# Kernel tuning notes

Hardware: AMD Instinct MI355X
Metric: run time of the kernel (lower is better)

## Reference

```python
import jax, jax.numpy as jnp
import numpy as np

V, D, NL, NC = 16, 256, 4, 2
MAXL, NSTATE, DCONV, EXPAND, HEADDIM = 1024, 64, 4, 2, 64
DIN = EXPAND * D            # 512 inner channels
H = DIN // HEADDIM          # 8 heads
P = HEADDIM                 # 64 head dim
CONV_DIM = DIN + 2 * NSTATE # 640 channels through depthwise conv
D_IN_PROJ = 2 * DIN + 2 * NSTATE + H  # 1160
B_, L_ = 2, 1024
EPS = 1e-5


def setup_inputs() -> dict:
    key = jax.random.key(0)
    ks = iter(jax.random.split(key, 32))

    def rn(shape, s=0.02):
        return jax.random.normal(next(ks), shape, jnp.float32) * s

    emb = rn((V, D)).at[4].set(0.0)  # padding_idx=4 row zeroed
    pos_emb = rn((MAXL, D))
    in_proj_w = rn((NL, D_IN_PROJ, D))
    conv_w = rn((NL, CONV_DIM, DCONV), 0.1)
    conv_b = rn((NL, CONV_DIM), 0.1)
    dt_bias = rn((NL, H), 0.5)
    A_log = jnp.log(jax.random.uniform(next(ks), (NL, H), jnp.float32, 1.0, 16.0))
    D_param = jnp.ones((NL, H), jnp.float32)
    norm_w = jnp.ones((NL, DIN), jnp.float32)
    out_proj_w = rn((NL, D, DIN))
    pooler_w = rn((D, D), 0.05)
    pooler_b = jnp.zeros((D,), jnp.float32)
    cls1_w = rn((D // 2, D), 0.05)
    cls1_b = jnp.zeros((D // 2,), jnp.float32)
    cls2_w = rn((NC, D // 2), 0.05)
    cls2_b = jnp.zeros((NC,), jnp.float32)
    input_ids = jax.random.randint(next(ks), (B_, L_), 0, V)
    return dict(input_ids=input_ids, emb=emb, pos_emb=pos_emb,
                in_proj_w=in_proj_w, conv_w=conv_w, conv_b=conv_b,
                dt_bias=dt_bias, A_log=A_log, D_param=D_param, norm_w=norm_w,
                out_proj_w=out_proj_w, pooler_w=pooler_w, pooler_b=pooler_b,
                cls1_w=cls1_w, cls1_b=cls1_b, cls2_w=cls2_w, cls2_b=cls2_b)


def _mamba2(x, Win, cw, cb, dtb, A_log, Dp, nw, Wout):
    Bsz, L, _ = x.shape
    zxbcdt = jnp.einsum('bld,pd->blp', x, Win)              # (B,L,2*DIN+2N+H)
    z = zxbcdt[..., :DIN]
    xBC = zxbcdt[..., DIN:DIN + CONV_DIM]
    dt = jax.nn.softplus(zxbcdt[..., -H:] + dtb)            # (B,L,H)
    # causal depthwise conv over time
    xBC = jnp.transpose(xBC, (0, 2, 1))                     # (B,C,L)
    xBC = jax.lax.conv_general_dilated(
        xBC, cw[:, None, :], (1,), [(DCONV - 1, 0)],
        dimension_numbers=('NCH', 'OIH', 'NCH'),
        feature_group_count=CONV_DIM)
    xBC = jax.nn.silu(jnp.transpose(xBC, (0, 2, 1)) + cb)   # (B,L,C)
    xs = xBC[..., :DIN].reshape(Bsz, L, H, P)
    Bm = xBC[..., DIN:DIN + NSTATE]                         # (B,L,N)
    Cm = xBC[..., DIN + NSTATE:]                            # (B,L,N)
    A = -jnp.exp(A_log)                                     # (H,)
    dA = jnp.exp(dt * A)                                    # (B,L,H)
    dBx = dt[..., None, None] * xs[..., None] * Bm[:, :, None, None, :]  # (B,L,H,P,N)

    def step(h, inp):
        dA_t, dBx_t, C_t = inp
        h = dA_t[:, :, None, None] * h + dBx_t              # (B,H,P,N)
        y = jnp.einsum('bhpn,bn->bhp', h, C_t)
        return h, y

    h0 = jnp.zeros((Bsz, H, P, NSTATE), x.dtype)
    _, y = jax.lax.scan(step, h0, (jnp.moveaxis(dA, 1, 0),
                                   jnp.moveaxis(dBx, 1, 0),
                                   jnp.moveaxis(Cm, 1, 0)))
    y = jnp.moveaxis(y, 0, 1) + Dp[None, None, :, None] * xs  # (B,L,H,P)
    y = y.reshape(Bsz, L, DIN) * jax.nn.silu(z)               # gated
    y = y * jax.lax.rsqrt(jnp.mean(y * y, axis=-1, keepdims=True) + EPS) * nw
    return jnp.einsum('bld,od->blo', y, Wout)


def reference(input_ids, emb, pos_emb, in_proj_w, conv_w, conv_b, dt_bias,
              A_log, D_param, norm_w, out_proj_w, pooler_w, pooler_b,
              cls1_w, cls1_b, cls2_w, cls2_b):
    L = input_ids.shape[1]
    x = emb[input_ids] + pos_emb[:L][None]                  # (B,L,D)
    for i in range(NL):
        x = x + _mamba2(x, in_proj_w[i], conv_w[i], conv_b[i], dt_bias[i],
                        A_log[i], D_param[i], norm_w[i], out_proj_w[i])
    pooled = (x.mean(axis=1) + x.max(axis=1)) * 0.5         # (B,D)
    pooled = jax.nn.gelu(pooled @ pooler_w.T + pooler_b, approximate=False)
    hcls = jax.nn.gelu(pooled @ cls1_w.T + cls1_b, approximate=False)
    return hcls @ cls2_w.T + cls2_b
```

## Files before the change

### kernel.cpp

```cpp
#include <hip/hip_runtime.h>
#include <math.h>

#define D_ 256
#define NL_ 4
#define NC_ 2
#define L_LEN 1024
#define NSTATE_ 64
#define DIN_ 512
#define H_ 8
#define P_ 64
#define CONVDIM_ 640
#define DPROJ_ 1160
#define EPS_ 1e-5f
#define NCH_ 16

typedef __attribute__((ext_vector_type(8))) short short8;
typedef __attribute__((ext_vector_type(4))) float f32x4;
typedef __attribute__((ext_vector_type(4))) unsigned short us4;

__device__ __forceinline__ float siluf(float x) { return x / (1.f + __expf(-x)); }
__device__ __forceinline__ float geluf(float x) { return 0.5f * x * (1.f + erff(x * 0.70710678118654752f)); }
__device__ __forceinline__ unsigned short f2bf(float f) {
    unsigned u = __float_as_uint(f);
    u += 0x7FFFu + ((u >> 16) & 1u);
    return (unsigned short)(u >> 16);
}
__device__ __forceinline__ float bf2f(unsigned short h) {
    return __uint_as_float(((unsigned)h) << 16);
}

__global__ void k_embed(const int* __restrict__ ids, const float* __restrict__ emb,
                        const float* __restrict__ pos, float* __restrict__ x, int total) {
    int i = blockIdx.x * blockDim.x + threadIdx.x;
    if (i >= total) return;
    int d = i & (D_ - 1);
    int bl = i >> 8;
    int l = bl & (L_LEN - 1);
    x[i] = emb[ids[bl] * D_ + d] + pos[l * D_ + d];
}

__global__ void k_w2bf2(const float* __restrict__ Wi, const float* __restrict__ Wo,
                        const float* __restrict__ nw,
                        unsigned short* __restrict__ wih, unsigned short* __restrict__ wil,
                        unsigned short* __restrict__ woh, unsigned short* __restrict__ wol,
                        int nin, int ntot) {
    int i = blockIdx.x * blockDim.x + threadIdx.x;
    if (i >= ntot) return;
    if (i < nin) {
        float f = Wi[i];
        unsigned short h = f2bf(f);
        wih[i] = h;
        wil[i] = f2bf(f - bf2f(h));
    } else {
        int j = i - nin;
        int layer = j / (D_ * DIN_);
        int k = j % DIN_;
        float f = Wo[j] * nw[layer * DIN_ + k];
        unsigned short h = f2bf(f);
        woh[j] = h;
        wol[j] = f2bf(f - bf2f(h));
    }
}

__global__ void __launch_bounds__(256) gemm_in(const float* __restrict__ A,
        const unsigned short* __restrict__ Bhi, const unsigned short* __restrict__ Blo,
        float* __restrict__ C, int M, int N, int K) {
    __shared__ __align__(16) unsigned short Ah[128 * 40];
    __shared__ __align__(16) unsigned short Al[128 * 40];
    __shared__ __align__(16) unsigned short Bh[64 * 40];
    __shared__ __align__(16) unsigned short Bl[64 * 40];
    const int tid = threadIdx.x;
    const int col0 = blockIdx.x * 64;
    const int row0 = blockIdx.y * 128;

    const int sar = tid >> 1, sas = (tid & 1) * 16;
    const int sbr = tid >> 2, sbs = (tid & 3) * 8;
    const bool bok = (col0 + sbr) < N;
    const float* aptr = A + (size_t)(row0 + sar) * K + sas;
    const unsigned short* bhptr = Bhi + (size_t)(col0 + sbr) * K + sbs;
    const unsigned short* blptr = Blo + (size_t)(col0 + sbr) * K + sbs;

    float4 pa[4];
    short8 pbh = {0, 0, 0, 0, 0, 0, 0, 0}, pbl = {0, 0, 0, 0, 0, 0, 0, 0};
#pragma unroll
    for (int i = 0; i < 4; ++i) pa[i] = *(const float4*)(aptr + i * 4);
    if (bok) {
        pbh = *(const short8*)bhptr;
        pbl = *(const short8*)blptr;
    }

    const int wave = tid >> 6, lane = tid & 63;
    const int lq = lane >> 4, lm = lane & 15;
    f32x4 acc[2][4] = {};
    const int nsteps = K >> 5;
    for (int s = 0; s < nsteps; ++s) {
        __syncthreads();
#pragma unroll
        for (int i = 0; i < 4; ++i) {
            float4 f = pa[i];
            unsigned short h0 = f2bf(f.x), h1 = f2bf(f.y), h2 = f2bf(f.z), h3 = f2bf(f.w);
            us4 hv = {h0, h1, h2, h3};
            us4 lv = {f2bf(f.x - bf2f(h0)), f2bf(f.y - bf2f(h1)),
                      f2bf(f.z - bf2f(h2)), f2bf(f.w - bf2f(h3))};
            *(us4*)&Ah[sar * 40 + sas + i * 4] = hv;
            *(us4*)&Al[sar * 40 + sas + i * 4] = lv;
        }
        *(short8*)&Bh[sbr * 40 + sbs] = pbh;
        *(short8*)&Bl[sbr * 40 + sbs] = pbl;
        __syncthreads();
        if (s + 1 < nsteps) {
            int ko = (s + 1) * 32;
#pragma unroll
            for (int i = 0; i < 4; ++i) pa[i] = *(const float4*)(aptr + ko + i * 4);
            if (bok) {
                pbh = *(const short8*)(bhptr + ko);
                pbl = *(const short8*)(blptr + ko);
            }
        }
        short8 bh[4], bl[4];
#pragma unroll
        for (int ct = 0; ct < 4; ++ct) {
            bh[ct] = *(const short8*)&Bh[(ct * 16 + lm) * 40 + lq * 8];
            bl[ct] = *(const short8*)&Bl[(ct * 16 + lm) * 40 + lq * 8];
        }
#pragma unroll
        for (int rt = 0; rt < 2; ++rt) {
            short8 ah = *(const short8*)&Ah[(wave * 32 + rt * 16 + lm) * 40 + lq * 8];
            short8 al = *(const short8*)&Al[(wave * 32 + rt * 16 + lm) * 40 + lq * 8];
#pragma unroll
            for (int ct = 0; ct < 4; ++ct) {
                acc[rt][ct] = __builtin_amdgcn_mfma_f32_16x16x32_bf16(ah, bh[ct], acc[rt][ct], 0, 0, 0);
                acc[rt][ct] = __builtin_amdgcn_mfma_f32_16x16x32_bf16(ah, bl[ct], acc[rt][ct], 0, 0, 0);
                acc[rt][ct] = __builtin_amdgcn_mfma_f32_16x16x32_bf16(al, bh[ct], acc[rt][ct], 0, 0, 0);
            }
        }
    }
#pragma unroll
    for (int rt = 0; rt < 2; ++rt) {
#pragma unroll
        for (int ct = 0; ct < 4; ++ct) {
            int col = col0 + ct * 16 + lm;
            if (col >= N) continue;
            int rbase = row0 + wave * 32 + rt * 16 + lq * 4;
#pragma unroll
            for (int reg = 0; reg < 4; ++reg) {
                C[(size_t)(rbase + reg) * N + col] = acc[rt][ct][reg];
            }
        }
    }
}

__global__ void __launch_bounds__(256) gemm_outs(const unsigned short* __restrict__ Ghg,
        const unsigned short* __restrict__ Glg, const float* __restrict__ rowssq,
        const unsigned short* __restrict__ Bhi, const unsigned short* __restrict__ Blo,
        float* __restrict__ x) {
    __shared__ __align__(16) unsigned short Ah[128 * 40];
    __shared__ __align__(16) unsigned short Al[128 * 40];
    __shared__ __align__(16) unsigned short Bh[64 * 40];
    __shared__ __align__(16) unsigned short Bl[64 * 40];
    const int tid = threadIdx.x;
    const int col0 = blockIdx.x * 64;
    const int row0 = blockIdx.y * 128;
    const int kbase = blockIdx.z * 128;
    const int sar = tid >> 1, sas = (tid & 1) * 16;
    const int sbr = tid >> 2, sbs = (tid & 3) * 8;
    const unsigned short* ahptr = Ghg + (size_t)(row0 + sar) * DIN_ + kbase + sas;
    const unsigned short* alptr = Glg + (size_t)(row0 + sar) * DIN_ + kbase + sas;
    const unsigned short* bhptr = Bhi + (size_t)(col0 + sbr) * DIN_ + kbase + sbs;
    const unsigned short* blptr = Blo + (size_t)(col0 + sbr) * DIN_ + kbase + sbs;

    short8 pah0 = *(const short8*)ahptr, pah1 = *(const short8*)(ahptr + 8);
    short8 pal0 = *(const short8*)alptr, pal1 = *(const short8*)(alptr + 8);
    short8 pbh = *(const short8*)bhptr, pbl = *(const short8*)blptr;

    const int wave = tid >> 6, lane = tid & 63;
    const int lq = lane >> 4, lm = lane & 15;
    f32x4 acc[2][4] = {};
    for (int s = 0; s < 4; ++s) {
        __syncthreads();
        *(short8*)&Ah[sar * 40 + sas] = pah0;
        *(short8*)&Ah[sar * 40 + sas + 8] = pah1;
        *(short8*)&Al[sar * 40 + sas] = pal0;
        *(short8*)&Al[sar * 40 + sas + 8] = pal1;
        *(short8*)&Bh[sbr * 40 + sbs] = pbh;
        *(short8*)&Bl[sbr * 40 + sbs] = pbl;
        __syncthreads();
        if (s + 1 < 4) {
            int ko = (s + 1) * 32;
            pah0 = *(const short8*)(ahptr + ko);
            pah1 = *(const short8*)(ahptr + ko + 8);
            pal0 = *(const short8*)(alptr + ko);
            pal1 = *(const short8*)(alptr + ko + 8);
            pbh = *(const short8*)(bhptr + ko);
            pbl = *(const short8*)(blptr + ko);
        }
        short8 bh[4], bl[4];
#pragma unroll
        for (int ct = 0; ct < 4; ++ct) {
            bh[ct] = *(const short8*)&Bh[(ct * 16 + lm) * 40 + lq * 8];
            bl[ct] = *(const short8*)&Bl[(ct * 16 + lm) * 40 + lq * 8];
        }
#pragma unroll
        for (int rt = 0; rt < 2; ++rt) {
            short8 ah = *(const short8*)&Ah[(wave * 32 + rt * 16 + lm) * 40 + lq * 8];
            short8 al = *(const short8*)&Al[(wave * 32 + rt * 16 + lm) * 40 + lq * 8];
#pragma unroll
            for (int ct = 0; ct < 4; ++ct) {
                acc[rt][ct] = __builtin_amdgcn_mfma_f32_16x16x32_bf16(ah, bh[ct], acc[rt][ct], 0, 0, 0);
                acc[rt][ct] = __builtin_amdgcn_mfma_f32_16x16x32_bf16(ah, bl[ct], acc[rt][ct], 0, 0, 0);
                acc[rt][ct] = __builtin_amdgcn_mfma_f32_16x16x32_bf16(al, bh[ct], acc[rt][ct], 0, 0, 0);
            }
        }
    }
#pragma unroll
    for (int rt = 0; rt < 2; ++rt) {
        int rbase = row0 + wave * 32 + rt * 16 + lq * 4;
        float sc[4];
#pragma unroll
        for (int reg = 0; reg < 4; ++reg)
            sc[reg] = rsqrtf(rowssq[rbase + reg] * (1.f / DIN_) + EPS_);
#pragma unroll
        for (int ct = 0; ct < 4; ++ct) {
            int col = col0 + ct * 16 + lm;
#pragma unroll
            for (int reg = 0; reg < 4; ++reg) {
                atomicAdd(&x[(size_t)(rbase + reg) * D_ + col], sc[reg] * acc[rt][ct][reg]);
            }
        }
    }
}

__global__ void __launch_bounds__(512) k_ssmA(const float* __restrict__ zx,
        const float* __restrict__ cw, const float* __restrict__ cb,
        const float* __restrict__ dtbias, const float* __restrict__ Alog,
        const float* __restrict__ Dp,
        float* __restrict__ Sbuf, float* __restrict__ decay,
        float* __restrict__ Ctil, float* __restrict__ y, float* __restrict__ rowssq) {
    __shared__ float U[64][65];
    __shared__ float V[64][65];
    __shared__ float W[64][65];
    __shared__ float sdt[64], cs[64], wj[64];
    const int c = blockIdx.x, bh = blockIdx.y;
    const int b = bh >> 3, h = bh & 7;
    const int l0 = c << 6;
    const int tid = threadIdx.x, wid8 = tid >> 6, lane = tid & 63;

    if (h == 0 && tid < 64) rowssq[b * L_LEN + l0 + tid] = 0.f;

    const int chx = h * P_ + lane;
    const int chb = DIN_ + lane;
    const int chc = DIN_ + NSTATE_ + lane;
    float wx0 = cw[chx * 4], wx1 = cw[chx * 4 + 1], wx2 = cw[chx * 4 + 2], wx3 = cw[chx * 4 + 3];
    float wb0 = cw[chb * 4], wb1 = cw[chb * 4 + 1], wb2 = cw[chb * 4 + 2], wb3 = cw[chb * 4 + 3];
    float wc0 = cw[chc * 4], wc1 = cw[chc * 4 + 1], wc2 = cw[chc * 4 + 2], wc3 = cw[chc * 4 + 3];
    float bx = cb[chx], bb = cb[chb], bc = cb[chc];

    for (int r = 0; r < 64; r += 8) {
        int j = r + wid8;
        int l = l0 + j;
        float ax = bx, ab = bb, ac = bc;
#pragma unroll
        for (int k = 0; k < 4; ++k) {
            int t = l - 3 + k;
            if (t >= 0) {
                const float* row = zx + (size_t)(b * L_LEN + t) * DPROJ_;
                float wxk = (k == 0) ? wx0 : (k == 1) ? wx1 : (k == 2) ? wx2 : wx3;
                float wbk = (k == 0) ? wb0 : (k == 1) ? wb1 : (k == 2) ? wb2 : wb3;
                float wck = (k == 0) ? wc0 : (k == 1) ? wc1 : (k == 2) ? wc2 : wc3;
                ax += wxk * row[DIN_ + chx];
                ab += wbk * row[DIN_ + chb];
                ac += wck * row[DIN_ + chc];
            }
        }
        U[j][lane] = siluf(ax);
        V[j][lane] = siluf(ab);
        W[j][lane] = siluf(ac);
    }
    if (tid < 64) {
        float xv = zx[(size_t)(b * L_LEN + l0 + tid) * DPROJ_ + (DPROJ_ - H_) + h] + dtbias[h];
        float sp = fmaxf(xv, 0.f) + log1pf(__expf(-fabsf(xv)));
        sdt[tid] = sp;
        float v = sp * (-__expf(Alog[h]));
#pragma unroll
        for (int off = 1; off < 64; off <<= 1) {
            float t = __shfl_up(v, off, 64);
            if (tid >= off) v += t;
        }
        cs[tid] = v;
        float tot = __shfl(v, 63, 64);
        wj[tid] = __expf(tot - v) * sp;
        if (tid == 63) decay[bh * NCH_ + c] = __expf(tot);
    }
    __syncthreads();

    const int t4 = (tid & 15) * 4;
    const int r4 = ((tid >> 4) & 15) * 4;
    const size_t sbase = (size_t)(bh * NCH_ + c) * 4096;

    if (tid < 256) {
        float acc[4][4] = {};
        for (int j = 0; j < 64; ++j) {
            float w = wj[j];
            float4 xv = *(const float4*)&U[j][r4];
            float4 bv = *(const float4*)&V[j][t4];
            float xw[4] = {xv.x * w, xv.y * w, xv.z * w, xv.w * w};
#pragma unroll
            for (int ii = 0; ii < 4; ++ii) {
                acc[ii][0] += xw[ii] * bv.x;
                acc[ii][1] += xw[ii] * bv.y;
                acc[ii][2] += xw[ii] * bv.z;
                acc[ii][3] += xw[ii] * bv.w;
            }
        }
#pragma unroll
        for (int ii = 0; ii < 4; ++ii) {
            float4 v = {acc[ii][0], acc[ii][1], acc[ii][2], acc[ii][3]};
            *(float4*)&Sbuf[sbase + (size_t)(r4 + ii) * 64 + t4] = v;
        }
    }
    for (int r = 0; r < 64; r += 8) {
        int ii = r + wid8;
        Ctil[sbase + ii * 64 + lane] = __expf(cs[ii]) * W[ii][lane];
    }
    float wt[4][4];
    if (tid < 256) {
        float g[4][4] = {};
        for (int ng = 0; ng < 64; ng += 4) {
            float4 cf[4], bf[4];
#pragma unroll
            for (int ii = 0; ii < 4; ++ii) cf[ii] = *(const float4*)&W[r4 + ii][ng];
#pragma unroll
            for (int jj = 0; jj < 4; ++jj) bf[jj] = *(const float4*)&V[t4 + jj][ng];
#pragma unroll
            for (int ii = 0; ii < 4; ++ii)
#pragma unroll
                for (int jj = 0; jj < 4; ++jj)
                    g[ii][jj] += cf[ii].x * bf[jj].x + cf[ii].y * bf[jj].y +
                                 cf[ii].z * bf[jj].z + cf[ii].w * bf[jj].w;
        }
#pragma unroll
        for (int ii = 0; ii < 4; ++ii) {
            int i = r4 + ii;
            float csi = cs[i];
#pragma unroll
            for (int jj = 0; jj < 4; ++jj) {
                int j = t4 + jj;
                wt[ii][jj] = (j <= i) ? __expf(fminf(csi - cs[j], 0.f)) * sdt[j] * g[ii][jj] : 0.f;
            }
        }
    }
    __syncthreads();
    if (tid < 256) {
#pragma unroll
        for (int jj = 0; jj < 4; ++jj) {
            float4 v = {wt[0][jj], wt[1][jj], wt[2][jj], wt[3][jj]};
            *(float4*)&V[t4 + jj][r4] = v;
        }
    }
    __syncthreads();
    if (tid < 256) {
        float acc[4][4] = {};
        for (int j = 0; j < 64; ++j) {
            float4 wv = *(const float4*)&V[j][r4];
            float4 xv = *(const float4*)&U[j][t4];
            float ws[4] = {wv.x, wv.y, wv.z, wv.w};
#pragma unroll
            for (int ii = 0; ii < 4; ++ii) {
                acc[ii][0] += ws[ii] * xv.x;
                acc[ii][1] += ws[ii] * xv.y;
                acc[ii][2] += ws[ii] * xv.z;
                acc[ii][3] += ws[ii] * xv.w;
            }
        }
        float Dh = Dp[h];
#pragma unroll
        for (int ii = 0; ii < 4; ++ii) {
            float4 xv = *(const float4*)&U[r4 + ii][t4];
            float4 v = {acc[ii][0] + Dh * xv.x, acc[ii][1] + Dh * xv.y,
                        acc[ii][2] + Dh * xv.z, acc[ii][3] + Dh * xv.w};
            *(float4*)&y[(size_t)(b * L_LEN + l0 + r4 + ii) * DIN_ + h * P_ + t4] = v;
        }
    }
}

__global__ void __launch_bounds__(512) k_inter(const float* __restrict__ Sbuf,
        const float* __restrict__ Ctil, const float* __restrict__ decay,
        const float* __restrict__ zx, const float* __restrict__ y,
        unsigned short* __restrict__ gh, unsigned short* __restrict__ gl,
        float* __restrict__ rowssq) {
    __shared__ float Sm[64][65];
    __shared__ float Cm[64][65];
    const int c = blockIdx.x, bh = blockIdx.y;
    const int b = bh >> 3, h = bh & 7;
    const int l0 = c << 6;
    const int tid = threadIdx.x, wid8 = tid >> 6, lane = tid & 63;
    const size_t bhbase = (size_t)bh * NCH_ * 4096;

    float dec[NCH_];
#pragma unroll
    for (int k = 0; k < NCH_; ++k) dec[k] = decay[bh * NCH_ + k];

    float acc8[8] = {};
    float wgt = 1.f;
    for (int cp = c - 1; cp >= 0; --cp) {
        const float* src = Sbuf + bhbase + (size_t)cp * 4096;
#pragma unroll
        for (int i = 0; i < 8; ++i) acc8[i] += wgt * src[i * 512 + tid];
        wgt *= dec[cp];
    }
#pragma unroll
    for (int i = 0; i < 8; ++i) Sm[i * 8 + wid8][lane] = acc8[i];

    const size_t base = bhbase + (size_t)c * 4096;
    for (int r = 0; r < 64; r += 8) {
        int pp = r + wid8;
        Cm[pp][lane] = Ctil[base + pp * 64 + lane];
    }
    __syncthreads();
    const int t4 = (tid & 15) * 4;
    const int r4 = ((tid >> 4) & 15) * 4;
    if (tid < 256) {
        float acc[4][4] = {};
        if (c > 0) {
            for (int ng = 0; ng < 64; ng += 4) {
                float4 cf[4], sf[4];
#pragma unroll
                for (int ii = 0; ii < 4; ++ii) cf[ii] = *(const float4*)&Cm[r4 + ii][ng];
#pragma unroll
                for (int pp = 0; pp < 4; ++pp) sf[pp] = *(const float4*)&Sm[t4 + pp][ng];
#pragma unroll
                for (int ii = 0; ii < 4; ++ii)
#pragma unroll
                    for (int pp = 0; pp < 4; ++pp)
                        acc[ii][pp] += cf[ii].x * sf[pp].x + cf[ii].y * sf[pp].y +
                                       cf[ii].z * sf[pp].z + cf[ii].w * sf[pp].w;
            }
        }
        float ssq[4];
#pragma unroll
        for (int ii = 0; ii < 4; ++ii) {
            int row = b * L_LEN + l0 + r4 + ii;
            const float* yr = &y[(size_t)row * DIN_ + h * P_ + t4];
            const float* zr = &zx[(size_t)row * DPROJ_ + h * P_ + t4];
            float4 v = *(const float4*)yr;
            float4 z = *(const float4*)zr;
            v.x = (v.x + acc[ii][0]) * siluf(z.x);
            v.y = (v.y + acc[ii][1]) * siluf(z.y);
            v.z = (v.z + acc[ii][2]) * siluf(z.z);
            v.w = (v.w + acc[ii][3]) * siluf(z.w);
            unsigned short h0 = f2bf(v.x), h1 = f2bf(v.y), h2 = f2bf(v.z), h3 = f2bf(v.w);
            us4 hv = {h0, h1, h2, h3};
            us4 lv = {f2bf(v.x - bf2f(h0)), f2bf(v.y - bf2f(h1)),
                      f2bf(v.z - bf2f(h2)), f2bf(v.w - bf2f(h3))};
            *(us4*)&gh[(size_t)row * DIN_ + h * P_ + t4] = hv;
            *(us4*)&gl[(size_t)row * DIN_ + h * P_ + t4] = lv;
            ssq[ii] = v.x * v.x + v.y * v.y + v.z * v.z + v.w * v.w;
        }
#pragma unroll
        for (int o = 1; o < 16; o <<= 1) {
#pragma unroll
            for (int ii = 0; ii < 4; ++ii) ssq[ii] += __shfl_xor(ssq[ii], o, 64);
        }
        if ((tid & 15) == 0) {
#pragma unroll
            for (int ii = 0; ii < 4; ++ii)
                atomicAdd(&rowssq[b * L_LEN + l0 + r4 + ii], ssq[ii]);
        }
    }
}

__global__ void __launch_bounds__(1024) k_poolhead(const float* __restrict__ x,
                           const float* __restrict__ pw, const float* __restrict__ pb,
                           const float* __restrict__ c1w, const float* __restrict__ c1b,
                           const float* __restrict__ c2w, const float* __restrict__ c2b,
                           float* __restrict__ out) {
    __shared__ float ps[4][256], pm[4][256];
    __shared__ float sp[256], s1[256], s2[128];
    int b = blockIdx.x, tid = threadIdx.x;
    int t = tid & 255, grp = tid >> 8;
    const float* xb = x + (size_t)b * L_LEN * D_ + (size_t)grp * 256 * D_ + t;
    float s = 0.f, m = -INFINITY;
    for (int l = 0; l < 256; l += 4) {
        float v0 = xb[(size_t)l * D_];
        float v1 = xb[(size_t)(l + 1) * D_];
        float v2 = xb[(size_t)(l + 2) * D_];
        float v3 = xb[(size_t)(l + 3) * D_];
        s += v0 + v1 + v2 + v3;
        m = fmaxf(m, fmaxf(fmaxf(v0, v1), fmaxf(v2, v3)));
    }
    ps[grp][t] = s;
    pm[grp][t] = m;
    __syncthreads();
    if (grp == 0) {
        float ss = ps[0][t] + ps[1][t] + ps[2][t] + ps[3][t];
        float mm = fmaxf(fmaxf(pm[0][t], pm[1][t]), fmaxf(pm[2][t], pm[3][t]));
        sp[t] = (ss * (1.f / L_LEN) + mm) * 0.5f;
    }
    __syncthreads();
    if (tid < 256) {
        float acc = pb[tid];
        for (int d = 0; d < 256; ++d) acc += sp[d] * pw[tid * 256 + d];
        s1[tid] = geluf(acc);
    }
    __syncthreads();
    if (tid < 128) {
        float a = c1b[tid];
        for (int d = 0; d < 256; ++d) a += s1[d] * c1w[tid * 256 + d];
        s2[tid] = geluf(a);
    }
    __syncthreads();
    if (tid < 2) {
        float a = c2b[tid];
        for (int d = 0; d < 128; ++d) a += s2[d] * c2w[tid * 128 + d];
        out[b * NC_ + tid] = a;
    }
}

extern "C" void kernel_launch(void* const* d_in, const int* in_sizes, int n_in,
                              void* d_out, int out_size, void* d_ws, size_t ws_size,
                              hipStream_t stream) {
    const int* ids    = (const int*)d_in[0];
    const float* emb  = (const float*)d_in[1];
    const float* pos  = (const float*)d_in[2];
    const float* Wins = (const float*)d_in[3];
    const float* cw   = (const float*)d_in[4];
    const float* cb   = (const float*)d_in[5];
    const float* dtb  = (const float*)d_in[6];
    const float* Alog = (const float*)d_in[7];
    const float* Dpar = (const float*)d_in[8];
    const float* nw   = (const float*)d_in[9];
    const float* Wout = (const float*)d_in[10];
    const float* pw   = (const float*)d_in[11];
    const float* pb   = (const float*)d_in[12];
    const float* c1w  = (const float*)d_in[13];
    const float* c1b  = (const float*)d_in[14];
    const float* c2w  = (const float*)d_in[15];
    const float* c2b  = (const float*)d_in[16];
    float* out = (float*)d_out;

    const int NWIN = NL_ * DPROJ_ * D_;
    const int NWOUT = NL_ * D_ * DIN_;
    const int NG = 1048576;

    float* ws = (float*)d_ws;
    float* x      = ws;
    float* zx     = x + 524288;
    float* y      = zx + 2375680;
    float* Sbuf   = y + 1048576;
    float* Ctil   = Sbuf + 1048576;
    float* decay  = Ctil + 1048576;
    float* rowssq = decay + 256;
    unsigned short* winh = (unsigned short*)(rowssq + 2048);
    unsigned short* winl = winh + NWIN;
    unsigned short* woh  = winl + NWIN;
    unsigned short* wol  = woh + NWOUT;
    unsigned short* gh   = wol + NWOUT;
    unsigned short* gl   = gh + NG;

    k_w2bf2<<<(NWIN + NWOUT + 255) / 256, 256, 0, stream>>>(
        Wins, Wout, nw, winh, winl, woh, wol, NWIN, NWIN + NWOUT);
    k_embed<<<2048, 256, 0, stream>>>(ids, emb, pos, x, 524288);
    for (int i = 0; i < NL_; ++i) {
        size_t wo_in = (size_t)i * DPROJ_ * D_;
        size_t wo_out = (size_t)i * D_ * DIN_;
        gemm_in<<<dim3(19, 16), 256, 0, stream>>>(
            x, winh + wo_in, winl + wo_in, zx, 2048, DPROJ_, D_);
        k_ssmA<<<dim3(NCH_, 16), 512, 0, stream>>>(
            zx, cw + (size_t)i * CONVDIM_ * 4, cb + (size_t)i * CONVDIM_,
            dtb + i * H_, Alog + i * H_, Dpar + i * H_, Sbuf, decay, Ctil, y, rowssq);
        k_inter<<<dim3(NCH_, 16), 512, 0, stream>>>(Sbuf, Ctil, decay, zx, y, gh, gl, rowssq);
        gemm_outs<<<dim3(4, 16, 4), 256, 0, stream>>>(
            gh, gl, rowssq, woh + wo_out, wol + wo_out, x);
    }
    k_poolhead<<<2, 1024, 0, stream>>>(x, pw, pb, c1w, c1b, c2w, c2b, out);
}
```

Before: 375.4 us.

## Precompute bf16 hi/lo split of activations before input projection GEMM

Moves the fp32-to-bf16 hi/lo split of the activation matrix out of gemm_in into the embedding kernel and a new per-layer conversion kernel. gemm_in then loads pre-split bf16 tiles directly, so each A element is no longer re-split by every one of the 19 column blocks. The cost is an extra small kernel launch per layer plus extra global traffic to write and read the split buffers. It also parallelizes the pooler and classifier matvecs across all threads with vectorized loads and shuffle reductions.

```diff
diff --git a/kernel.cpp b/kernel.cpp
--- a/kernel.cpp
+++ b/kernel.cpp
@@ -30,13 +30,32 @@
 }
 
 __global__ void k_embed(const int* __restrict__ ids, const float* __restrict__ emb,
-                        const float* __restrict__ pos, float* __restrict__ x, int total) {
+                        const float* __restrict__ pos, float* __restrict__ x,
+                        unsigned short* __restrict__ xh, unsigned short* __restrict__ xl,
+                        int total) {
     int i = blockIdx.x * blockDim.x + threadIdx.x;
     if (i >= total) return;
     int d = i & (D_ - 1);
     int bl = i >> 8;
     int l = bl & (L_LEN - 1);
-    x[i] = emb[ids[bl] * D_ + d] + pos[l * D_ + d];
+    float v = emb[ids[bl] * D_ + d] + pos[l * D_ + d];
+    x[i] = v;
+    unsigned short h = f2bf(v);
+    xh[i] = h;
+    xl[i] = f2bf(v - bf2f(h));
+}
+
+__global__ void k_x2bf(const float* __restrict__ x, unsigned short* __restrict__ xh,
+                       unsigned short* __restrict__ xl, int total4) {
+    int i = blockIdx.x * blockDim.x + threadIdx.x;
+    if (i >= total4) return;
+    float4 f = ((const float4*)x)[i];
+    unsigned short h0 = f2bf(f.x), h1 = f2bf(f.y), h2 = f2bf(f.z), h3 = f2bf(f.w);
+    us4 hv = {h0, h1, h2, h3};
+    us4 lv = {f2bf(f.x - bf2f(h0)), f2bf(f.y - bf2f(h1)),
+              f2bf(f.z - bf2f(h2)), f2bf(f.w - bf2f(h3))};
+    ((us4*)xh)[i] = hv;
+    ((us4*)xl)[i] = lv;
 }
 
 __global__ void k_w2bf2(const float* __restrict__ Wi, const float* __restrict__ Wo,
@@ -62,7 +81,8 @@
     }
 }
 
-__global__ void __launch_bounds__(256) gemm_in(const float* __restrict__ A,
+__global__ void __launch_bounds__(256) gemm_in(const unsigned short* __restrict__ Ahg,
+        const unsigned short* __restrict__ Alg,
         const unsigned short* __restrict__ Bhi, const unsigned short* __restrict__ Blo,
         float* __restrict__ C, int M, int N, int K) {
     __shared__ __align__(16) unsigned short Ah[128 * 40];
@@ -76,14 +96,14 @@
     const int sar = tid >> 1, sas = (tid & 1) * 16;
     const int sbr = tid >> 2, sbs = (tid & 3) * 8;
     const bool bok = (col0 + sbr) < N;
-    const float* aptr = A + (size_t)(row0 + sar) * K + sas;
+    const unsigned short* ahptr = Ahg + (size_t)(row0 + sar) * K + sas;
+    const unsigned short* alptr = Alg + (size_t)(row0 + sar) * K + sas;
     const unsigned short* bhptr = Bhi + (size_t)(col0 + sbr) * K + sbs;
     const unsigned short* blptr = Blo + (size_t)(col0 + sbr) * K + sbs;
 
-    float4 pa[4];
+    short8 pah0 = *(const short8*)ahptr, pah1 = *(const short8*)(ahptr + 8);
+    short8 pal0 = *(const short8*)alptr, pal1 = *(const short8*)(alptr + 8);
     short8 pbh = {0, 0, 0, 0, 0, 0, 0, 0}, pbl = {0, 0, 0, 0, 0, 0, 0, 0};
-#pragma unroll
-    for (int i = 0; i < 4; ++i) pa[i] = *(const float4*)(aptr + i * 4);
     if (bok) {
         pbh = *(const short8*)bhptr;
         pbl = *(const short8*)blptr;
@@ -95,23 +115,19 @@
     const int nsteps = K >> 5;
     for (int s = 0; s < nsteps; ++s) {
         __syncthreads();
-#pragma unroll
-        for (int i = 0; i < 4; ++i) {
-            float4 f = pa[i];
-            unsigned short h0 = f2bf(f.x), h1 = f2bf(f.y), h2 = f2bf(f.z), h3 = f2bf(f.w);
-            us4 hv = {h0, h1, h2, h3};
-            us4 lv = {f2bf(f.x - bf2f(h0)), f2bf(f.y - bf2f(h1)),
-                      f2bf(f.z - bf2f(h2)), f2bf(f.w - bf2f(h3))};
-            *(us4*)&Ah[sar * 40 + sas + i * 4] = hv;
-            *(us4*)&Al[sar * 40 + sas + i * 4] = lv;
-        }
+        *(short8*)&Ah[sar * 40 + sas] = pah0;
+        *(short8*)&Ah[sar * 40 + sas + 8] = pah1;
+        *(short8*)&Al[sar * 40 + sas] = pal0;
+        *(short8*)&Al[sar * 40 + sas + 8] = pal1;
         *(short8*)&Bh[sbr * 40 + sbs] = pbh;
         *(short8*)&Bl[sbr * 40 + sbs] = pbl;
         __syncthreads();
         if (s + 1 < nsteps) {
             int ko = (s + 1) * 32;
-#pragma unroll
-            for (int i = 0; i < 4; ++i) pa[i] = *(const float4*)(aptr + ko + i * 4);
+            pah0 = *(const short8*)(ahptr + ko);
+            pah1 = *(const short8*)(ahptr + ko + 8);
+            pal0 = *(const short8*)(alptr + ko);
+            pal1 = *(const short8*)(alptr + ko + 8);
             if (bok) {
                 pbh = *(const short8*)(bhptr + ko);
                 pbl = *(const short8*)(blptr + ko);
@@ -497,16 +513,35 @@
         sp[t] = (ss * (1.f / L_LEN) + mm) * 0.5f;
     }
     __syncthreads();
-    if (tid < 256) {
-        float acc = pb[tid];
-        for (int d = 0; d < 256; ++d) acc += sp[d] * pw[tid * 256 + d];
-        s1[tid] = geluf(acc);
-    }
-    __syncthreads();
-    if (tid < 128) {
-        float a = c1b[tid];
-        for (int d = 0; d < 256; ++d) a += s1[d] * c1w[tid * 256 + d];
-        s2[tid] = geluf(a);
+    {
+        int o = tid >> 2, part = tid & 3;
+        const float* wrow = pw + (size_t)o * 256 + part * 64;
+        const float* sv = sp + part * 64;
+        float acc = 0.f;
+        for (int d = 0; d < 64; d += 4) {
+            float4 w4 = *(const float4*)(wrow + d);
+            float4 x4 = *(const float4*)(sv + d);
+            acc += w4.x * x4.x + w4.y * x4.y + w4.z * x4.z + w4.w * x4.w;
+        }
+        acc += __shfl_xor(acc, 1, 64);
+        acc += __shfl_xor(acc, 2, 64);
+        if (part == 0) s1[o] = geluf(acc + pb[o]);
+    }
+    __syncthreads();
+    {
+        int o = tid >> 3, part = tid & 7;
+        const float* wrow = c1w + (size_t)o * 256 + part * 32;
+        const float* sv = s1 + part * 32;
+        float acc = 0.f;
+        for (int d = 0; d < 32; d += 4) {
+            float4 w4 = *(const float4*)(wrow + d);
+            float4 x4 = *(const float4*)(sv + d);
+            acc += w4.x * x4.x + w4.y * x4.y + w4.z * x4.z + w4.w * x4.w;
+        }
+        acc += __shfl_xor(acc, 1, 64);
+        acc += __shfl_xor(acc, 2, 64);
+        acc += __shfl_xor(acc, 4, 64);
+        if (part == 0) s2[o] = geluf(acc + c1b[o]);
     }
     __syncthreads();
     if (tid < 2) {
@@ -541,6 +576,7 @@
     const int NWIN = NL_ * DPROJ_ * D_;
     const int NWOUT = NL_ * D_ * DIN_;
     const int NG = 1048576;
+    const int NX = 524288;
 
     float* ws = (float*)d_ws;
     float* x      = ws;
@@ -556,21 +592,26 @@
     unsigned short* wol  = woh + NWOUT;
     unsigned short* gh   = wol + NWOUT;
     unsigned short* gl   = gh + NG;
+    unsigned short* xh   = gl + NG;
+    unsigned short* xl   = xh + NX;
 
     k_w2bf2<<<(NWIN + NWOUT + 255) / 256, 256, 0, stream>>>(
         Wins, Wout, nw, winh, winl, woh, wol, NWIN, NWIN + NWOUT);
-    k_embed<<<2048, 256, 0, stream>>>(ids, emb, pos, x, 524288);
+    k_embed<<<2048, 256, 0, stream>>>(ids, emb, pos, x, xh, xl, NX);
     for (int i = 0; i < NL_; ++i) {
         size_t wo_in = (size_t)i * DPROJ_ * D_;
         size_t wo_out = (size_t)i * D_ * DIN_;
         gemm_in<<<dim3(19, 16), 256, 0, stream>>>(
-            x, winh + wo_in, winl + wo_in, zx, 2048, DPROJ_, D_);
+            xh, xl, winh + wo_in, winl + wo_in, zx, 2048, DPROJ_, D_);
         k_ssmA<<<dim3(NCH_, 16), 512, 0, stream>>>(
             zx, cw + (size_t)i * CONVDIM_ * 4, cb + (size_t)i * CONVDIM_,
             dtb + i * H_, Alog + i * H_, Dpar + i * H_, Sbuf, decay, Ctil, y, rowssq);
         k_inter<<<dim3(NCH_, 16), 512, 0, stream>>>(Sbuf, Ctil, decay, zx, y, gh, gl, rowssq);
         gemm_outs<<<dim3(4, 16, 4), 256, 0, stream>>>(
             gh, gl, rowssq, woh + wo_out, wol + wo_out, x);
+        if (i + 1 < NL_) {
+            k_x2bf<<<(NX / 4 + 255) / 256, 256, 0, stream>>>(x, xh, xl, NX / 4);
+        }
     }
     k_poolhead<<<2, 1024, 0, stream>>>(x, pw, pb, c1w, c1b, c2w, c2b, out);
 }
```

New measurement: 377.0 us. Within noise of the previous version (+0.4%).
